# Kernel tuning notes

Hardware: AMD Instinct MI355X
Metric: run time of the kernel (lower is better)

Reference implementation:

```python
import jax, jax.numpy as jnp
import numpy as np

G = 512      # number of structures (groups)
CNT = 8192   # residues per structure
S = 8192     # sampled pairs per structure (self.samples)
N = G * CNT  # total residues


def _sample_pairs():
    # Deterministic replication of StochasticRGNLoss.pairs: per-group randint
    # sampling, with group offsets added so indices address the global array.
    rng = np.random.default_rng(0)
    local = rng.integers(0, CNT, size=(G, S, 2))
    # avoid degenerate left==right pairs (zero distance -> NaN grad of norm)
    eq = local[..., 0] == local[..., 1]
    local[..., 1] = np.where(eq, (local[..., 1] + 1) % CNT, local[..., 1])
    offs = (np.arange(G) * CNT)[:, None, None]
    pairs = (local + offs).reshape(-1, 2)
    return pairs[:, 0].astype(np.int32), pairs[:, 1].astype(np.int32)


def setup_inputs() -> dict:
    key = jax.random.key(0)
    k1, k2 = jax.random.split(key)
    inputs = jax.random.normal(k1, (N, 3, 3), dtype=jnp.float32)
    target = jax.random.normal(k2, (N, 3, 3), dtype=jnp.float32)
    left_np, right_np = _sample_pairs()
    return {
        "inputs": inputs,
        "target": target,
        "left": jnp.asarray(left_np),
        "right": jnp.asarray(right_np),
    }


def reference(inputs, target, left, right):
    # take the CA atom (index 1) of each residue frame -> [N, 3]
    ca_in = inputs[:, 1]
    ca_tg = target[:, 1]
    # irregular gather of sampled pairs, pairwise distances -> [P]
    d_in = jnp.linalg.norm(ca_in[left] - ca_in[right], axis=1)
    d_tg = jnp.linalg.norm(ca_tg[left] - ca_tg[right], axis=1)
    return jnp.mean((d_in - d_tg) ** 2)
```

## Files before the change

### kernel.cpp

```cpp
#include <hip/hip_runtime.h>

#define G_GROUPS 512
#define CNT      8192
#define S_PAIRS  8192
#define BLOCK    1024
#define WAVES    (BLOCK / 64)
#define PPT      (S_PAIRS / BLOCK)
#define RPT      (CNT / BLOCK)

__global__ __launch_bounds__(BLOCK) void rgn_loss_kernel(
    const float* __restrict__ inputs,
    const float* __restrict__ target,
    const int*   __restrict__ left,
    const int*   __restrict__ right,
    float*       __restrict__ out)
{
    __shared__ float4 tab4[CNT];
    __shared__ float  red[WAVES];

    const int tid   = threadIdx.x;
    const int lane  = tid & 63;
    const int wid   = tid >> 6;
    const int g     = blockIdx.x;
    const int gbase = g * CNT;

    const size_t pbase = (size_t)g * S_PAIRS;
    int li[PPT], ri[PPT];
    #pragma unroll
    for (int i = 0; i < PPT; ++i) {
        li[i] = left [pbase + tid + i * BLOCK] - gbase;
        ri[i] = right[pbase + tid + i * BLOCK] - gbase;
    }

    float4 iv[RPT];
    #pragma unroll
    for (int k = 0; k < RPT; ++k) {
        const float* p = inputs + (size_t)(gbase + tid + k * BLOCK) * 9 + 3;
        __builtin_memcpy(&iv[k], p, 16);
    }
    #pragma unroll
    for (int k = 0; k < RPT; ++k)
        tab4[tid + k * BLOCK] = iv[k];
    __syncthreads();

    float4 tv[RPT];
    #pragma unroll
    for (int k = 0; k < RPT; ++k) {
        const float* p = target + (size_t)(gbase + tid + k * BLOCK) * 9 + 3;
        __builtin_memcpy(&tv[k], p, 16);
    }
    asm volatile("" ::: "memory");

    float din[PPT];
    #pragma unroll
    for (int i = 0; i < PPT; ++i) {
        const float4 L = tab4[li[i]];
        const float4 R = tab4[ri[i]];
        const float dx = L.x - R.x;
        const float dy = L.y - R.y;
        const float dz = L.z - R.z;
        din[i] = sqrtf(dx * dx + dy * dy + dz * dz);
    }
    __syncthreads();

    #pragma unroll
    for (int k = 0; k < RPT; ++k)
        tab4[tid + k * BLOCK] = tv[k];
    __syncthreads();

    float acc = 0.0f;
    #pragma unroll
    for (int i = 0; i < PPT; ++i) {
        const float4 L = tab4[li[i]];
        const float4 R = tab4[ri[i]];
        const float dx = L.x - R.x;
        const float dy = L.y - R.y;
        const float dz = L.z - R.z;
        const float d  = din[i] - sqrtf(dx * dx + dy * dy + dz * dz);
        acc += d * d;
    }

    #pragma unroll
    for (int off = 32; off > 0; off >>= 1)
        acc += __shfl_down(acc, off);
    if (lane == 0) red[wid] = acc;
    __syncthreads();
    if (wid == 0) {
        float v = (lane < WAVES) ? red[lane] : 0.0f;
        #pragma unroll
        for (int off = 8; off > 0; off >>= 1)
            v += __shfl_down(v, off);
        if (lane == 0)
            atomicAdd(out, v * (1.0f / ((float)G_GROUPS * (float)S_PAIRS)));
    }
}

extern "C" void kernel_launch(void* const* d_in, const int* in_sizes, int n_in,
                              void* d_out, int out_size, void* d_ws, size_t ws_size,
                              hipStream_t stream) {
    const float* inputs = (const float*)d_in[0];
    const float* target = (const float*)d_in[1];
    const int*   left   = (const int*)d_in[2];
    const int*   right  = (const int*)d_in[3];
    float*       out    = (float*)d_out;

    hipMemsetAsync(out, 0, sizeof(float), stream);
    rgn_loss_kernel<<<G_GROUPS, BLOCK, 0, stream>>>(inputs, target, left, right, out);
}
```

Baseline: 348.7 us.

## Replace LDS-staged residue tables with direct global gathers and XCD-aware block mapping

Drops the per-group shared-memory staging of CA coordinates and instead gathers the needed input and target coordinates directly from global memory for each sampled pair. The grid becomes many smaller 256-thread blocks, each handling a slice of pairs, with block IDs remapped so consecutive pairs of a group land on the same XCD to improve L2 reuse. This removes the barrier-heavy staging and the large LDS footprint that limited occupancy. In exchange, it relies on caches to absorb the random, partially wasted gather traffic.

```diff
diff --git a/kernel.cpp b/kernel.cpp
--- a/kernel.cpp
+++ b/kernel.cpp
@@ -3,10 +3,12 @@
 #define G_GROUPS 512
 #define CNT      8192
 #define S_PAIRS  8192
-#define BLOCK    1024
+#define BLOCK    256
 #define WAVES    (BLOCK / 64)
-#define PPT      (S_PAIRS / BLOCK)
-#define RPT      (CNT / BLOCK)
+#define PPT      16
+#define PAIRS_PER_BLOCK (BLOCK * PPT)
+#define NWG      ((G_GROUPS * S_PAIRS) / PAIRS_PER_BLOCK)
+#define NXCD     8
 
 __global__ __launch_bounds__(BLOCK) void rgn_loss_kernel(
     const float* __restrict__ inputs,
@@ -15,69 +17,54 @@
     const int*   __restrict__ right,
     float*       __restrict__ out)
 {
-    __shared__ float4 tab4[CNT];
-    __shared__ float  red[WAVES];
+    __shared__ float red[WAVES];
 
-    const int tid   = threadIdx.x;
-    const int lane  = tid & 63;
-    const int wid   = tid >> 6;
-    const int g     = blockIdx.x;
-    const int gbase = g * CNT;
+    const int tid  = threadIdx.x;
+    const int lane = tid & 63;
+    const int wid  = tid >> 6;
 
-    const size_t pbase = (size_t)g * S_PAIRS;
+    const int p   = blockIdx.x;
+    const int b   = (p % NXCD) * (NWG / NXCD) + p / NXCD;
+
+    const size_t pbase = (size_t)b * PAIRS_PER_BLOCK;
+
     int li[PPT], ri[PPT];
     #pragma unroll
     for (int i = 0; i < PPT; ++i) {
-        li[i] = left [pbase + tid + i * BLOCK] - gbase;
-        ri[i] = right[pbase + tid + i * BLOCK] - gbase;
+        li[i] = left [pbase + tid + i * BLOCK];
+        ri[i] = right[pbase + tid + i * BLOCK];
     }
 
-    float4 iv[RPT];
-    #pragma unroll
-    for (int k = 0; k < RPT; ++k) {
-        const float* p = inputs + (size_t)(gbase + tid + k * BLOCK) * 9 + 3;
-        __builtin_memcpy(&iv[k], p, 16);
-    }
-    #pragma unroll
-    for (int k = 0; k < RPT; ++k)
-        tab4[tid + k * BLOCK] = iv[k];
-    __syncthreads();
-
-    float4 tv[RPT];
-    #pragma unroll
-    for (int k = 0; k < RPT; ++k) {
-        const float* p = target + (size_t)(gbase + tid + k * BLOCK) * 9 + 3;
-        __builtin_memcpy(&tv[k], p, 16);
-    }
-    asm volatile("" ::: "memory");
-
-    float din[PPT];
-    #pragma unroll
-    for (int i = 0; i < PPT; ++i) {
-        const float4 L = tab4[li[i]];
-        const float4 R = tab4[ri[i]];
-        const float dx = L.x - R.x;
-        const float dy = L.y - R.y;
-        const float dz = L.z - R.z;
-        din[i] = sqrtf(dx * dx + dy * dy + dz * dz);
-    }
-    __syncthreads();
-
-    #pragma unroll
-    for (int k = 0; k < RPT; ++k)
-        tab4[tid + k * BLOCK] = tv[k];
-    __syncthreads();
-
     float acc = 0.0f;
-    #pragma unroll
-    for (int i = 0; i < PPT; ++i) {
-        const float4 L = tab4[li[i]];
-        const float4 R = tab4[ri[i]];
-        const float dx = L.x - R.x;
-        const float dy = L.y - R.y;
-        const float dz = L.z - R.z;
-        const float d  = din[i] - sqrtf(dx * dx + dy * dy + dz * dz);
-        acc += d * d;
+    #pragma unroll 1
+    for (int c = 0; c < PPT / 2; ++c) {
+        float4 aL0, aR0, bL0, bR0, aL1, aR1, bL1, bR1;
+        {
+            const int l0 = li[2 * c], r0 = ri[2 * c];
+            const int l1 = li[2 * c + 1], r1 = ri[2 * c + 1];
+            __builtin_memcpy(&aL0, inputs + (size_t)l0 * 9 + 3, 16);
+            __builtin_memcpy(&aR0, inputs + (size_t)r0 * 9 + 3, 16);
+            __builtin_memcpy(&bL0, target + (size_t)l0 * 9 + 3, 16);
+            __builtin_memcpy(&bR0, target + (size_t)r0 * 9 + 3, 16);
+            __builtin_memcpy(&aL1, inputs + (size_t)l1 * 9 + 3, 16);
+            __builtin_memcpy(&aR1, inputs + (size_t)r1 * 9 + 3, 16);
+            __builtin_memcpy(&bL1, target + (size_t)l1 * 9 + 3, 16);
+            __builtin_memcpy(&bR1, target + (size_t)r1 * 9 + 3, 16);
+        }
+        {
+            const float dx = aL0.x - aR0.x, dy = aL0.y - aR0.y, dz = aL0.z - aR0.z;
+            const float ex = bL0.x - bR0.x, ey = bL0.y - bR0.y, ez = bL0.z - bR0.z;
+            const float d = sqrtf(dx * dx + dy * dy + dz * dz)
+                          - sqrtf(ex * ex + ey * ey + ez * ez);
+            acc += d * d;
+        }
+        {
+            const float dx = aL1.x - aR1.x, dy = aL1.y - aR1.y, dz = aL1.z - aR1.z;
+            const float ex = bL1.x - bR1.x, ey = bL1.y - bR1.y, ez = bL1.z - bR1.z;
+            const float d = sqrtf(dx * dx + dy * dy + dz * dz)
+                          - sqrtf(ex * ex + ey * ey + ez * ez);
+            acc += d * d;
+        }
     }
 
     #pragma unroll
@@ -85,13 +72,9 @@
         acc += __shfl_down(acc, off);
     if (lane == 0) red[wid] = acc;
     __syncthreads();
-    if (wid == 0) {
-        float v = (lane < WAVES) ? red[lane] : 0.0f;
-        #pragma unroll
-        for (int off = 8; off > 0; off >>= 1)
-            v += __shfl_down(v, off);
-        if (lane == 0)
-            atomicAdd(out, v * (1.0f / ((float)G_GROUPS * (float)S_PAIRS)));
+    if (wid == 0 && lane == 0) {
+        float v = red[0] + red[1] + red[2] + red[3];
+        atomicAdd(out, v * (1.0f / ((float)G_GROUPS * (float)S_PAIRS)));
     }
 }
 
@@ -105,5 +88,5 @@
     float*       out    = (float*)d_out;
 
     hipMemsetAsync(out, 0, sizeof(float), stream);
-    rgn_loss_kernel<<<G_GROUPS, BLOCK, 0, stream>>>(inputs, target, left, right, out);
+    rgn_loss_kernel<<<NWG, BLOCK, 0, stream>>>(inputs, target, left, right, out);
 }
```

After: 451.8 us. +29.6%, slower.

## Process two groups per workgroup with software-pipelined global loads

Applied to the files above, without the earlier changes.

Each workgroup now handles two structures one after the other, so only half as many workgroups are launched. Global loads for the next table (target of group A, inputs of group B, target of group B) and group B's pair indices are issued before the LDS gather of the current table, which hides load latency behind gather work. Barriers are replaced with a custom LDS-wait plus s_barrier, and launch bounds request more waves per SIMD. The cost is more registers in flight and fewer workgroups, which may leave CUs underused with 256 blocks on a 256-CU part.

```diff
diff --git a/kernel.cpp b/kernel.cpp
--- a/kernel.cpp
+++ b/kernel.cpp
@@ -6,9 +6,55 @@
 #define BLOCK    1024
 #define WAVES    (BLOCK / 64)
 #define PPT      (S_PAIRS / BLOCK)
-#define RPT      (CNT / BLOCK)
+#define GPB      2
+#define NWG      (G_GROUPS / GPB)
 
-__global__ __launch_bounds__(BLOCK) void rgn_loss_kernel(
+#define LOADCA(dst, src, rec)                                         \
+    __builtin_memcpy(&(dst), (src) + (size_t)(rec) * 9 + 3, 16)
+
+#define LOAD8(p, SRC, GB)                                             \
+    float4 p##0, p##1, p##2, p##3, p##4, p##5, p##6, p##7;            \
+    LOADCA(p##0, SRC, (GB) + tid + 0 * BLOCK);                        \
+    LOADCA(p##1, SRC, (GB) + tid + 1 * BLOCK);                        \
+    LOADCA(p##2, SRC, (GB) + tid + 2 * BLOCK);                        \
+    LOADCA(p##3, SRC, (GB) + tid + 3 * BLOCK);                        \
+    LOADCA(p##4, SRC, (GB) + tid + 4 * BLOCK);                        \
+    LOADCA(p##5, SRC, (GB) + tid + 5 * BLOCK);                        \
+    LOADCA(p##6, SRC, (GB) + tid + 6 * BLOCK);                        \
+    LOADCA(p##7, SRC, (GB) + tid + 7 * BLOCK);
+
+#define WRITE8(p)                                                     \
+    tab4[tid + 0 * BLOCK] = p##0;  tab4[tid + 1 * BLOCK] = p##1;      \
+    tab4[tid + 2 * BLOCK] = p##2;  tab4[tid + 3 * BLOCK] = p##3;      \
+    tab4[tid + 4 * BLOCK] = p##4;  tab4[tid + 5 * BLOCK] = p##5;      \
+    tab4[tid + 6 * BLOCK] = p##6;  tab4[tid + 7 * BLOCK] = p##7;
+
+#define GATH_DIN(LI, RI)                                              \
+    _Pragma("unroll")                                                 \
+    for (int i = 0; i < PPT; ++i) {                                   \
+        const float4 L = tab4[LI[i]];                                 \
+        const float4 R = tab4[RI[i]];                                 \
+        const float dx = L.x - R.x, dy = L.y - R.y, dz = L.z - R.z;   \
+        din[i] = sqrtf(dx * dx + dy * dy + dz * dz);                  \
+    }
+
+#define GATH_DTG(LI, RI)                                              \
+    _Pragma("unroll")                                                 \
+    for (int i = 0; i < PPT; ++i) {                                   \
+        const float4 L = tab4[LI[i]];                                 \
+        const float4 R = tab4[RI[i]];                                 \
+        const float dx = L.x - R.x, dy = L.y - R.y, dz = L.z - R.z;   \
+        const float d  = din[i] - sqrtf(dx * dx + dy * dy + dz * dz); \
+        acc += d * d;                                                 \
+    }
+
+__device__ __forceinline__ void fencebar() {
+    asm volatile("s_waitcnt lgkmcnt(0)" ::: "memory");
+    __builtin_amdgcn_s_barrier();
+    asm volatile("" ::: "memory");
+}
+
+__global__ __launch_bounds__(BLOCK, 4) void rgn_loss_kernel(
     const float* __restrict__ inputs,
     const float* __restrict__ target,
     const int*   __restrict__ left,
@@ -18,67 +64,62 @@
     __shared__ float4 tab4[CNT];
     __shared__ float  red[WAVES];
 
-    const int tid   = threadIdx.x;
-    const int lane  = tid & 63;
-    const int wid   = tid >> 6;
-    const int g     = blockIdx.x;
-    const int gbase = g * CNT;
+    const int tid = threadIdx.x;
+    const int lane = tid & 63;
+    const int wid  = tid >> 6;
 
-    const size_t pbase = (size_t)g * S_PAIRS;
-    int li[PPT], ri[PPT];
-    #pragma unroll
-    for (int i = 0; i < PPT; ++i) {
-        li[i] = left [pbase + tid + i * BLOCK] - gbase;
-        ri[i] = right[pbase + tid + i * BLOCK] - gbase;
-    }
-
-    float4 iv[RPT];
-    #pragma unroll
-    for (int k = 0; k < RPT; ++k) {
-        const float* p = inputs + (size_t)(gbase + tid + k * BLOCK) * 9 + 3;
-        __builtin_memcpy(&iv[k], p, 16);
-    }
-    #pragma unroll
-    for (int k = 0; k < RPT; ++k)
-        tab4[tid + k * BLOCK] = iv[k];
-    __syncthreads();
-
-    float4 tv[RPT];
-    #pragma unroll
-    for (int k = 0; k < RPT; ++k) {
-        const float* p = target + (size_t)(gbase + tid + k * BLOCK) * 9 + 3;
-        __builtin_memcpy(&tv[k], p, 16);
-    }
-    asm volatile("" ::: "memory");
+    const int gA = blockIdx.x * GPB;
+    const int gB = gA + 1;
+    const int baseA = gA * CNT;
+    const int baseB = gB * CNT;
 
     float din[PPT];
-    #pragma unroll
-    for (int i = 0; i < PPT; ++i) {
-        const float4 L = tab4[li[i]];
-        const float4 R = tab4[ri[i]];
-        const float dx = L.x - R.x;
-        const float dy = L.y - R.y;
-        const float dz = L.z - R.z;
-        din[i] = sqrtf(dx * dx + dy * dy + dz * dz);
+    float acc = 0.0f;
+
+    int ali[PPT], ari[PPT];
+    {
+        const size_t pb = (size_t)gA * S_PAIRS;
+        #pragma unroll
+        for (int i = 0; i < PPT; ++i) {
+            ali[i] = left [pb + tid + i * BLOCK] - baseA;
+            ari[i] = right[pb + tid + i * BLOCK] - baseA;
+        }
     }
-    __syncthreads();
+    LOAD8(av, inputs, baseA)
+    WRITE8(av)
+    fencebar();
 
-    #pragma unroll
-    for (int k = 0; k < RPT; ++k)
-        tab4[tid + k * BLOCK] = tv[k];
-    __syncthreads();
+    LOAD8(at, target, baseA)
+    GATH_DIN(ali, ari)
+    fencebar();
 
-    float acc = 0.0f;
-    #pragma unroll
-    for (int i = 0; i < PPT; ++i) {
-        const float4 L = tab4[li[i]];
-        const float4 R = tab4[ri[i]];
-        const float dx = L.x - R.x;
-        const float dy = L.y - R.y;
-        const float dz = L.z - R.z;
-        const float d  = din[i] - sqrtf(dx * dx + dy * dy + dz * dz);
-        acc += d * d;
+    WRITE8(at)
+    fencebar();
+
+    LOAD8(bv, inputs, baseB)
+    int bli[PPT], bri[PPT];
+    {
+        const size_t pb = (size_t)gB * S_PAIRS;
+        #pragma unroll
+        for (int i = 0; i < PPT; ++i) {
+            bli[i] = left [pb + tid + i * BLOCK] - baseB;
+            bri[i] = right[pb + tid + i * BLOCK] - baseB;
+        }
     }
+    GATH_DTG(ali, ari)
+    fencebar();
+
+    WRITE8(bv)
+    fencebar();
+
+    LOAD8(bt, target, baseB)
+    GATH_DIN(bli, bri)
+    fencebar();
+
+    WRITE8(bt)
+    fencebar();
+
+    GATH_DTG(bli, bri)
 
     #pragma unroll
     for (int off = 32; off > 0; off >>= 1)
@@ -105,5 +146,5 @@
     float*       out    = (float*)d_out;
 
     hipMemsetAsync(out, 0, sizeof(float), stream);
-    rgn_loss_kernel<<<G_GROUPS, BLOCK, 0, stream>>>(inputs, target, left, right, out);
+    rgn_loss_kernel<<<NWG, BLOCK, 0, stream>>>(inputs, target, left, right, out);
 }
```

Result: faster. 330.9 us (-5.1%).

## Stage CA table via split direct-to-LDS and register loads across waves

Applied to the files above, without the earlier changes.

Each coordinate table is now filled in two halves. Half the waves use global_load_lds to move data straight into LDS, and the other half load through registers and store to LDS. The old prefetch of target into registers is dropped, so target loading is no longer overlapped with the inputs distance pass. Launch bounds now request 4 waves per EU. The goal is to cut register pressure and VGPR staging traffic, at the cost of losing that overlap and relying on hand-written waitcnt and barrier sequences.

```diff
diff --git a/kernel.cpp b/kernel.cpp
--- a/kernel.cpp
+++ b/kernel.cpp
@@ -6,9 +6,57 @@
 #define BLOCK    1024
 #define WAVES    (BLOCK / 64)
 #define PPT      (S_PAIRS / BLOCK)
-#define RPT      (CNT / BLOCK)
+#define HALF     (CNT / 2)
 
-__global__ __launch_bounds__(BLOCK) void rgn_loss_kernel(
+typedef __attribute__((address_space(3))) void  lds_void;
+typedef const __attribute__((address_space(1))) void g_void;
+
+#define LOADCA(dst, src, rec)                                         \
+    __builtin_memcpy(&(dst), (src) + (size_t)(rec) * 9 + 3, 16)
+
+#define DUAL_STAGE(SRC)                                                       \
+    if (wid < 8) {                                                            \
+        const int rb = wid * 512;                                             \
+        _Pragma("unroll")                                                     \
+        for (int c = 0; c < 8; ++c) {                                         \
+            const int r = rb + c * 64;             \
+            const float* gp = (SRC) + (size_t)(gbase + r + lane) * 9 + 3;     \
+            __builtin_amdgcn_global_load_lds((g_void*)gp,                     \
+                                             (lds_void*)&tab4[r], 16, 0, 0);  \
+        }                                                                     \
+        asm volatile("s_waitcnt vmcnt(0)" ::: "memory");                      \
+    } else {                                                                  \
+        const int vt = tid - 512;                \
+        const int vb = gbase + HALF + vt;                                     \
+        float4 v0, v1, v2, v3, v4, v5, v6, v7;                                \
+        LOADCA(v0, SRC, vb + 0 * 512);                                        \
+        LOADCA(v1, SRC, vb + 1 * 512);                                        \
+        LOADCA(v2, SRC, vb + 2 * 512);                                        \
+        LOADCA(v3, SRC, vb + 3 * 512);                                        \
+        LOADCA(v4, SRC, vb + 4 * 512);                                        \
+        LOADCA(v5, SRC, vb + 5 * 512);                                        \
+        LOADCA(v6, SRC, vb + 6 * 512);                                        \
+        LOADCA(v7, SRC, vb + 7 * 512);                                        \
+        tab4[HALF + vt + 0 * 512] = v0;                                       \
+        tab4[HALF + vt + 1 * 512] = v1;                                       \
+        tab4[HALF + vt + 2 * 512] = v2;                                       \
+        tab4[HALF + vt + 3 * 512] = v3;                                       \
+        tab4[HALF + vt + 4 * 512] = v4;                                       \
+        tab4[HALF + vt + 5 * 512] = v5;                                       \
+        tab4[HALF + vt + 6 * 512] = v6;                                       \
+        tab4[HALF + vt + 7 * 512] = v7;                                       \
+        asm volatile("s_waitcnt lgkmcnt(0)" ::: "memory");                    \
+    }                                                                         \
+    __builtin_amdgcn_s_barrier();                                             \
+    asm volatile("" ::: "memory");
+
+__device__ __forceinline__ void fencebar() {
+    asm volatile("s_waitcnt lgkmcnt(0)" ::: "memory");
+    __builtin_amdgcn_s_barrier();
+    asm volatile("" ::: "memory");
+}
+
+__global__ __launch_bounds__(BLOCK, 4) void rgn_loss_kernel(
     const float* __restrict__ inputs,
     const float* __restrict__ target,
     const int*   __restrict__ left,
@@ -32,50 +80,26 @@
         ri[i] = right[pbase + tid + i * BLOCK] - gbase;
     }
 
-    float4 iv[RPT];
-    #pragma unroll
-    for (int k = 0; k < RPT; ++k) {
-        const float* p = inputs + (size_t)(gbase + tid + k * BLOCK) * 9 + 3;
-        __builtin_memcpy(&iv[k], p, 16);
-    }
-    #pragma unroll
-    for (int k = 0; k < RPT; ++k)
-        tab4[tid + k * BLOCK] = iv[k];
-    __syncthreads();
-
-    float4 tv[RPT];
-    #pragma unroll
-    for (int k = 0; k < RPT; ++k) {
-        const float* p = target + (size_t)(gbase + tid + k * BLOCK) * 9 + 3;
-        __builtin_memcpy(&tv[k], p, 16);
-    }
-    asm volatile("" ::: "memory");
+    DUAL_STAGE(inputs)
 
     float din[PPT];
     #pragma unroll
     for (int i = 0; i < PPT; ++i) {
         const float4 L = tab4[li[i]];
         const float4 R = tab4[ri[i]];
-        const float dx = L.x - R.x;
-        const float dy = L.y - R.y;
-        const float dz = L.z - R.z;
+        const float dx = L.x - R.x, dy = L.y - R.y, dz = L.z - R.z;
         din[i] = sqrtf(dx * dx + dy * dy + dz * dz);
     }
-    __syncthreads();
+    fencebar();
 
-    #pragma unroll
-    for (int k = 0; k < RPT; ++k)
-        tab4[tid + k * BLOCK] = tv[k];
-    __syncthreads();
+    DUAL_STAGE(target)
 
     float acc = 0.0f;
     #pragma unroll
     for (int i = 0; i < PPT; ++i) {
         const float4 L = tab4[li[i]];
         const float4 R = tab4[ri[i]];
-        const float dx = L.x - R.x;
-        const float dy = L.y - R.y;
-        const float dz = L.z - R.z;
+        const float dx = L.x - R.x, dy = L.y - R.y, dz = L.z - R.z;
         const float d  = din[i] - sqrtf(dx * dx + dy * dy + dz * dz);
         acc += d * d;
     }
```

Result: faster. 332.7 us (-4.6%).
